# Kernel tuning notes

Hardware: AMD Instinct MI355X
Metric: run time of the kernel (lower is better)

Reference implementation:

```python
import jax, jax.numpy as jnp
import numpy as np

EMBED_DIM = 1024
NUM_HEADS = 16
HEAD_DIM = EMBED_DIM // NUM_HEADS
B, S = 2, 2048


def setup_inputs() -> dict:
    key = jax.random.key(0)
    ks = jax.random.split(key, 11)
    sc = 1.0 / np.sqrt(EMBED_DIM)
    d = {
        'query': jax.random.normal(ks[0], (B, S, EMBED_DIM), jnp.float32),
        'key': jax.random.normal(ks[1], (B, S, EMBED_DIM), jnp.float32),
        'value': jax.random.normal(ks[2], (B, S, EMBED_DIM), jnp.float32),
        'Wq': jax.random.normal(ks[3], (EMBED_DIM, EMBED_DIM), jnp.float32) * sc,
        'bq': jnp.zeros((EMBED_DIM,), jnp.float32),
        'Wk': jax.random.normal(ks[4], (EMBED_DIM, EMBED_DIM), jnp.float32) * sc,
        'bk': jnp.zeros((EMBED_DIM,), jnp.float32),
        'Wv': jax.random.normal(ks[5], (EMBED_DIM, EMBED_DIM), jnp.float32) * sc,
        'bv': jnp.zeros((EMBED_DIM,), jnp.float32),
        'Wo': jax.random.normal(ks[6], (EMBED_DIM, EMBED_DIM), jnp.float32) * sc,
        'bo': jnp.zeros((EMBED_DIM,), jnp.float32),
    }
    return d


def reference(query, key, value, Wq, bq, Wk, bk, Wv, bv, Wo, bo):
    b, s, _ = query.shape
    scale = 1.0 / np.sqrt(HEAD_DIM)
    # projections: torch Linear is x @ W.T + b
    q = (query @ Wq.T + bq).reshape(b, s, NUM_HEADS, HEAD_DIM).transpose(0, 2, 1, 3)
    k = (key @ Wk.T + bk).reshape(b, s, NUM_HEADS, HEAD_DIM).transpose(0, 2, 1, 3)
    v = (value @ Wv.T + bv).reshape(b, s, NUM_HEADS, HEAD_DIM).transpose(0, 2, 1, 3)
    scores = jnp.einsum('bhqd,bhkd->bhqk', q, k) * scale  # [B,H,S,S]
    causal = jnp.triu(jnp.ones((s, s), bool), k=1)
    scores = jnp.where(causal, -jnp.inf, scores)
    attn = jax.nn.softmax(scores, axis=-1)
    out = jnp.einsum('bhqk,bhkd->bhqd', attn, v)
    out = out.transpose(0, 2, 1, 3).reshape(b, s, EMBED_DIM)
    out = out @ Wo.T + bo
    return out, attn
```

## Files before the change

### kernel.cpp

```cpp
#include <hip/hip_runtime.h>
#include <hip/hip_bf16.h>

#define BATCH  2
#define SEQ    2048
#define EMBED  1024
#define NHEADS 16
#define HDIM   64
#define SCALE  0.125f
#define S2     0.180336880f
#define MFIX   20.0f
#define PPITCH 72

typedef __attribute__((ext_vector_type(8))) short   short8;
typedef __attribute__((ext_vector_type(4))) float   floatx4;

#if __has_builtin(__builtin_amdgcn_exp2f)
#define EXP2(x) __builtin_amdgcn_exp2f(x)
#else
#define EXP2(x) exp2f(x)
#endif

#define GLOAD_LDS(g, l) __builtin_amdgcn_global_load_lds(                      \
    (const __attribute__((address_space(1))) void*)(const void*)(g),           \
    (__attribute__((address_space(3))) void*)(void*)(l), 16, 0, 0)

__device__ __forceinline__ float bf2f(unsigned short h) {
    union { unsigned int u; float f; } v; v.u = ((unsigned int)h) << 16; return v.f;
}
__device__ __forceinline__ unsigned short f2bf(float f) {
    union { float f; unsigned int u; } v; v.f = f;
    unsigned int r = v.u + 0x7FFF + ((v.u >> 16) & 1);
    return (unsigned short)(r >> 16);
}
__device__ __forceinline__ unsigned int pack2(float lo, float hi) {
    return (unsigned int)f2bf(lo) | ((unsigned int)f2bf(hi) << 16);
}

__device__ __forceinline__ void bar_lds() {
    __builtin_amdgcn_sched_barrier(0);
    asm volatile("s_waitcnt lgkmcnt(0)" ::: "memory");
    __builtin_amdgcn_s_barrier();
    __builtin_amdgcn_sched_barrier(0);
}

__global__ __launch_bounds__(256)
void cvt_bf16(const float* __restrict__ q,  const float* __restrict__ k,
              const float* __restrict__ v,  const float* __restrict__ wq,
              const float* __restrict__ wk, const float* __restrict__ wv,
              const float* __restrict__ wo,
              unsigned short* __restrict__ dq,  unsigned short* __restrict__ dk,
              unsigned short* __restrict__ dv,  unsigned short* __restrict__ dwq,
              unsigned short* __restrict__ dwk, unsigned short* __restrict__ dwv,
              unsigned short* __restrict__ dwo)
{
    const float* s; unsigned short* d; int n;
    switch (blockIdx.y) {
        case 0: s = q;  d = dq;  n = BATCH * SEQ * EMBED; break;
        case 1: s = k;  d = dk;  n = BATCH * SEQ * EMBED; break;
        case 2: s = v;  d = dv;  n = BATCH * SEQ * EMBED; break;
        case 3: s = wq; d = dwq; n = EMBED * EMBED; break;
        case 4: s = wk; d = dwk; n = EMBED * EMBED; break;
        case 5: s = wv; d = dwv; n = EMBED * EMBED; break;
        default: s = wo; d = dwo; n = EMBED * EMBED; break;
    }
    const int i = (blockIdx.x * 256 + threadIdx.x) * 8;
    if (i >= n) return;
    float4 f0 = ((const float4*)(s + i))[0];
    float4 f1 = ((const float4*)(s + i))[1];
    uint4 u = {pack2(f0.x, f0.y), pack2(f0.z, f0.w),
               pack2(f1.x, f1.y), pack2(f1.z, f1.w)};
    *(uint4*)(d + i) = u;
}

__device__ __forceinline__ void gemm_body(
    const unsigned short* __restrict__ A,
    const unsigned short* __restrict__ W,
    const float* __restrict__ bias,
    void* __restrict__ Cout, const int f32out,
    const int bx, const int by)
{
    constexpr int N = EMBED;
    constexpr int K = EMBED;

    __shared__ unsigned short As[2][128 * 64];
    __shared__ unsigned short Bs[2][64 * 64];

    const int t    = threadIdx.x;
    const int w    = t >> 6;
    const int lane = t & 63;
    const int lr   = lane & 15;
    const int quad = lane >> 4;
    const int n0   = bx * 64;
    const int m0   = by * 128;

    size_t agoff[4];
    #pragma unroll
    for (int i = 0; i < 4; ++i) {
        const int slot = i * 256 + w * 64 + lane;
        const int row  = slot >> 3;
        const int g    = (slot & 7) ^ (row & 7);
        agoff[i] = (size_t)(m0 + row) * K + g * 8;
    }
    size_t bgoff[2];
    #pragma unroll
    for (int i = 0; i < 2; ++i) {
        const int slot = i * 256 + w * 64 + lane;
        const int row  = slot >> 3;
        const int g    = (slot & 7) ^ (row & 7);
        bgoff[i] = (size_t)(n0 + row) * K + g * 8;
    }

    int aoff[2][2], boff[4][2];
    #pragma unroll
    for (int mb = 0; mb < 2; ++mb)
        #pragma unroll
        for (int s = 0; s < 2; ++s) {
            const int row = w * 32 + mb * 16 + lr;
            aoff[mb][s] = row * 64 + (((s * 4 + quad) ^ (row & 7)) * 8);
        }
    #pragma unroll
    for (int nb = 0; nb < 4; ++nb)
        #pragma unroll
        for (int s = 0; s < 2; ++s) {
            const int row = nb * 16 + lr;
            boff[nb][s] = row * 64 + (((s * 4 + quad) ^ (row & 7)) * 8);
        }

    floatx4 acc[2][4];
    #pragma unroll
    for (int mb = 0; mb < 2; ++mb)
        #pragma unroll
        for (int nb = 0; nb < 4; ++nb) acc[mb][nb] = (floatx4){0.f, 0.f, 0.f, 0.f};

    auto stage = [&](int buf, int k0) {
        #pragma unroll
        for (int i = 0; i < 4; ++i)
            GLOAD_LDS(A + agoff[i] + k0, &As[buf][(i * 256 + w * 64) * 8]);
        #pragma unroll
        for (int i = 0; i < 2; ++i)
            GLOAD_LDS(W + bgoff[i] + k0, &Bs[buf][(i * 256 + w * 64) * 8]);
    };
    auto compute = [&](int buf) {
        const unsigned short* Ab = As[buf];
        const unsigned short* Bb = Bs[buf];
        #pragma unroll
        for (int s = 0; s < 2; ++s) {
            short8 a0 = *(const short8*)&Ab[aoff[0][s]];
            short8 a1 = *(const short8*)&Ab[aoff[1][s]];
            #pragma unroll
            for (int nb = 0; nb < 4; ++nb) {
                short8 bfr = *(const short8*)&Bb[boff[nb][s]];
                acc[0][nb] = __builtin_amdgcn_mfma_f32_16x16x32_bf16(a0, bfr, acc[0][nb], 0, 0, 0);
                acc[1][nb] = __builtin_amdgcn_mfma_f32_16x16x32_bf16(a1, bfr, acc[1][nb], 0, 0, 0);
            }
        }
    };

    stage(0, 0);
    __syncthreads();
    for (int k0 = 0; k0 < K; k0 += 128) {
        if (k0 + 64 < K) stage(1, k0 + 64);
        compute(0);
        __syncthreads();
        if (k0 + 128 < K) stage(0, k0 + 128);
        compute(1);
        __syncthreads();
    }

    #pragma unroll
    for (int mb = 0; mb < 2; ++mb)
        #pragma unroll
        for (int nb = 0; nb < 4; ++nb) {
            const int col = n0 + nb * 16 + lr;
            const float bv = bias[col];
            #pragma unroll
            for (int r = 0; r < 4; ++r) {
                const int row = m0 + w * 32 + mb * 16 + quad * 4 + r;
                const float val = acc[mb][nb][r] + bv;
                if (f32out) ((float*)Cout)[(size_t)row * N + col] = val;
                else        ((unsigned short*)Cout)[(size_t)row * N + col] = f2bf(val);
            }
        }
}

__global__ __launch_bounds__(256)
void gemm_qkv(const unsigned short* __restrict__ xq, const unsigned short* __restrict__ xk,
              const unsigned short* __restrict__ xv,
              const unsigned short* __restrict__ wq, const unsigned short* __restrict__ wk,
              const unsigned short* __restrict__ wv,
              const float* __restrict__ bq, const float* __restrict__ bk,
              const float* __restrict__ bv,
              unsigned short* __restrict__ Qb, unsigned short* __restrict__ Kb,
              unsigned short* __restrict__ Vb)
{
    const unsigned short *A, *W; const float* bias; unsigned short* C;
    switch (blockIdx.z) {
        case 0:  A = xq; W = wq; bias = bq; C = Qb; break;
        case 1:  A = xk; W = wk; bias = bk; C = Kb; break;
        default: A = xv; W = wv; bias = bv; C = Vb; break;
    }
    gemm_body(A, W, bias, C, 0, blockIdx.x, blockIdx.y);
}

__global__ __launch_bounds__(256)
void attn_pass(const unsigned short* __restrict__ Qb,
               const unsigned short* __restrict__ Kb,
               const unsigned short* __restrict__ Vb,
               unsigned short* __restrict__ Pb,
               float* __restrict__ Lbuf,
               unsigned short* __restrict__ AO)
{
    __shared__ unsigned short Ks[2][64][PPITCH];
    __shared__ unsigned short Vt[2][64][PPITCH];
    __shared__ unsigned short Ps[64][PPITCH];

    const int t    = threadIdx.x;
    const int w    = t >> 6;
    const int lane = t & 63;
    const int lr   = lane & 15;
    const int quad = lane >> 4;
    const int h    = blockIdx.y;
    const int b    = blockIdx.z;
    const int slot = (h >> 3) + 2 * b;
    const int qt   = (slot & 1) ? (SEQ / 64 - 1 - (int)blockIdx.x) : (int)blockIdx.x;
    const int q0   = qt * 64;
    const int srow = t >> 2;
    const int sseg = (t & 3) * 16;
    const int bh   = b * NHEADS + h;

    const size_t kvbase = (size_t)b * SEQ * EMBED + h * HDIM;

    const unsigned short* qrow = Qb + kvbase + (size_t)(q0 + w * 16 + lr) * EMBED + quad * 8;
    const short8 af0 = *(const short8*)(qrow);
    const short8 af1 = *(const short8*)(qrow + 32);

    const unsigned short* Krow = Kb + kvbase + (size_t)srow * EMBED + sseg;
    const unsigned short* Vrow = Vb + kvbase + (size_t)lane * EMBED;

    uint4 kA0, kA1, vA0, vA1;
    uint4 kB0, kB1, vB0, vB1;

    kA0 = ((const uint4*)Krow)[0];
    kA1 = ((const uint4*)Krow)[1];
    vA0 = *(const uint4*)(Vrow + w * 8);
    vA1 = *(const uint4*)(Vrow + (w + 4) * 8);
    *(uint4*)&Ks[0][srow][sseg]     = kA0;
    *(uint4*)&Ks[0][srow][sseg + 8] = kA1;
    {
        const unsigned short* p0 = (const unsigned short*)&vA0;
        const unsigned short* p1 = (const unsigned short*)&vA1;
        #pragma unroll
        for (int j = 0; j < 8; ++j) Vt[0][w * 8 + j][lane]       = p0[j];
        #pragma unroll
        for (int j = 0; j < 8; ++j) Vt[0][(w + 4) * 8 + j][lane] = p1[j];
    }
    if (qt > 0) {
        const unsigned short* kp = Krow + (size_t)64 * EMBED;
        kB0 = ((const uint4*)kp)[0];
        kB1 = ((const uint4*)kp)[1];
        vB0 = *(const uint4*)(Vrow + (size_t)64 * EMBED + w * 8);
        vB1 = *(const uint4*)(Vrow + (size_t)64 * EMBED + (w + 4) * 8);
    }
    bar_lds();

    float lsum[4];
    #pragma unroll
    for (int r = 0; r < 4; ++r) lsum[r] = 0.f;
    floatx4 of[4];
    #pragma unroll
    for (int i = 0; i < 4; ++i) of[i] = (floatx4){0.f, 0.f, 0.f, 0.f};

    unsigned short* pb_bh = Pb + (size_t)bh * SEQ * (SEQ * 2);
    const int rrow = lane >> 2;
    const int rseg = (lane & 3) * 16;

    for (int kt = 0; kt <= qt; ++kt) {
        const int c  = kt & 1;
        const int k0 = kt * 64;

        if (kt < qt) {
            if ((kt & 1) == 0) {
                *(uint4*)&Ks[c ^ 1][srow][sseg]     = kB0;
                *(uint4*)&Ks[c ^ 1][srow][sseg + 8] = kB1;
                const unsigned short* p0 = (const unsigned short*)&vB0;
                const unsigned short* p1 = (const unsigned short*)&vB1;
                #pragma unroll
                for (int j = 0; j < 8; ++j) Vt[c ^ 1][w * 8 + j][lane]       = p0[j];
                #pragma unroll
                for (int j = 0; j < 8; ++j) Vt[c ^ 1][(w + 4) * 8 + j][lane] = p1[j];
                if (kt + 2 <= qt) {
                    const unsigned short* kp = Krow + (size_t)(k0 + 128) * EMBED;
                    kA0 = ((const uint4*)kp)[0];
                    kA1 = ((const uint4*)kp)[1];
                    vA0 = *(const uint4*)(Vrow + (size_t)(k0 + 128) * EMBED + w * 8);
                    vA1 = *(const uint4*)(Vrow + (size_t)(k0 + 128) * EMBED + (w + 4) * 8);
                }
            } else {
                *(uint4*)&Ks[c ^ 1][srow][sseg]     = kA0;
                *(uint4*)&Ks[c ^ 1][srow][sseg + 8] = kA1;
                const unsigned short* p0 = (const unsigned short*)&vA0;
                const unsigned short* p1 = (const unsigned short*)&vA1;
                #pragma unroll
                for (int j = 0; j < 8; ++j) Vt[c ^ 1][w * 8 + j][lane]       = p0[j];
                #pragma unroll
                for (int j = 0; j < 8; ++j) Vt[c ^ 1][(w + 4) * 8 + j][lane] = p1[j];
                if (kt + 2 <= qt) {
                    const unsigned short* kp = Krow + (size_t)(k0 + 128) * EMBED;
                    kB0 = ((const uint4*)kp)[0];
                    kB1 = ((const uint4*)kp)[1];
                    vB0 = *(const uint4*)(Vrow + (size_t)(k0 + 128) * EMBED + w * 8);
                    vB1 = *(const uint4*)(Vrow + (size_t)(k0 + 128) * EMBED + (w + 4) * 8);
                }
            }
        }

        floatx4 sf[4];
        #pragma unroll
        for (int i = 0; i < 4; ++i) sf[i] = (floatx4){0.f, 0.f, 0.f, 0.f};
        #pragma unroll
        for (int nb = 0; nb < 4; ++nb) {
            short8 bf0 = *(const short8*)&Ks[c][nb * 16 + lr][quad * 8];
            sf[nb] = __builtin_amdgcn_mfma_f32_16x16x32_bf16(af0, bf0, sf[nb], 0, 0, 0);
        }
        #pragma unroll
        for (int nb = 0; nb < 4; ++nb) {
            short8 bf1 = *(const short8*)&Ks[c][nb * 16 + lr][32 + quad * 8];
            sf[nb] = __builtin_amdgcn_mfma_f32_16x16x32_bf16(af1, bf1, sf[nb], 0, 0, 0);
        }

        if (kt < qt) {
            #pragma unroll
            for (int nb = 0; nb < 4; ++nb)
                #pragma unroll
                for (int r = 0; r < 4; ++r) {
                    float p = EXP2(sf[nb][r] * S2 - MFIX);
                    lsum[r] += p;
                    Ps[w * 16 + quad * 4 + r][nb * 16 + lr] = f2bf(p);
                }
        } else {
            #pragma unroll
            for (int nb = 0; nb < 4; ++nb) {
                const int k = nb * 16 + lr;
                #pragma unroll
                for (int r = 0; r < 4; ++r) {
                    const int q = w * 16 + quad * 4 + r;
                    float p = 0.f;
                    if (k <= q) { p = EXP2(sf[nb][r] * S2 - MFIX); lsum[r] += p; }
                    Ps[w * 16 + quad * 4 + r][nb * 16 + lr] = f2bf(p);
                }
            }
        }

        {
            const unsigned short* ps = &Ps[w * 16 + rrow][rseg];
            unsigned short* op = pb_bh + (size_t)(q0 + w * 16 + rrow) * (SEQ * 2) + k0 + rseg;
            *(uint4*)op       = *(const uint4*)ps;
            *(uint4*)(op + 8) = *(const uint4*)(ps + 8);
        }

        #pragma unroll
        for (int ss = 0; ss < 2; ++ss) {
            short8 paf = *(const short8*)&Ps[w * 16 + lr][ss * 32 + quad * 8];
            #pragma unroll
            for (int nb = 0; nb < 4; ++nb) {
                short8 vf = *(const short8*)&Vt[c][nb * 16 + lr][ss * 32 + quad * 8];
                of[nb] = __builtin_amdgcn_mfma_f32_16x16x32_bf16(paf, vf, of[nb], 0, 0, 0);
            }
        }

        bar_lds();
    }

    float invl[4];
    #pragma unroll
    for (int r = 0; r < 4; ++r) {
        #pragma unroll
        for (int off = 1; off < 16; off <<= 1)
            lsum[r] += __shfl_xor(lsum[r], off, 64);
        invl[r] = 1.f / lsum[r];
    }
    if (lr == 0) {
        #pragma unroll
        for (int r = 0; r < 4; ++r)
            Lbuf[(size_t)bh * SEQ + q0 + w * 16 + quad * 4 + r] = invl[r];
    }

    #pragma unroll
    for (int nb = 0; nb < 4; ++nb)
        #pragma unroll
        for (int r = 0; r < 4; ++r)
            Ps[w * 16 + quad * 4 + r][nb * 16 + lr] = f2bf(of[nb][r] * invl[r]);
    {
        unsigned short* ao = AO + (size_t)(b * SEQ + q0 + w * 16 + rrow) * EMBED + h * HDIM + rseg;
        *(uint4*)ao       = *(const uint4*)&Ps[w * 16 + rrow][rseg];
        *(uint4*)(ao + 8) = *(const uint4*)&Ps[w * 16 + rrow][rseg + 8];
    }
}

__global__ __launch_bounds__(256)
void out_norm(const unsigned short* __restrict__ AO, const unsigned short* __restrict__ Wo16,
              const float* __restrict__ bo, float* __restrict__ out,
              float* __restrict__ attn, const float* __restrict__ Lbuf)
{
    const int id = blockIdx.x;
    if (id < 512) {
        gemm_body(AO, Wo16, bo, out, 1, id & 15, id >> 4);
        return;
    }
    const int id2   = id - 512;
    const int bh    = id2 >> 5;
    const int x     = id2 & 31;
    const int chunk = (bh & 1) ? (31 - x) : x;
    const int t     = threadIdx.x;
    const int w     = t >> 6;
    const int lane  = t & 63;

    const unsigned short* pb = (const unsigned short*)(attn + (size_t)bh * SEQ * SEQ);
    float* ab = attn + (size_t)bh * SEQ * SEQ;

    for (int i = 0; i < 16; ++i) {
        const int q  = chunk * 64 + w * 16 + i;
        const int qc = (q & ~63) + 64;
        const float il = Lbuf[(size_t)bh * SEQ + q];
        const unsigned short* src = pb + (size_t)q * (SEQ * 2);
        float* dst = ab + (size_t)q * SEQ;

        uint4 rr[4];
        #pragma unroll
        for (int s = 0; s < 4; ++s) {
            const int c = lane * 8 + s * 512;
            if (c < qc) rr[s] = *(const uint4*)(src + c);
        }
        #pragma unroll
        for (int s = 0; s < 4; ++s) {
            const int c = lane * 8 + s * 512;
            if (c < qc) {
                const unsigned short* u = (const unsigned short*)&rr[s];
                float4 f0 = {bf2f(u[0]) * il, bf2f(u[1]) * il, bf2f(u[2]) * il, bf2f(u[3]) * il};
                float4 f1 = {bf2f(u[4]) * il, bf2f(u[5]) * il, bf2f(u[6]) * il, bf2f(u[7]) * il};
                ((float4*)(dst + c))[0] = f0;
                ((float4*)(dst + c))[1] = f1;
            }
        }
        for (int c = qc + lane * 8; c < SEQ; c += 512) {
            float4 z = {0.f, 0.f, 0.f, 0.f};
            ((float4*)(dst + c))[0] = z;
            ((float4*)(dst + c))[1] = z;
        }
    }
}

extern "C" void kernel_launch(void* const* d_in, const int* in_sizes, int n_in,
                              void* d_out, int out_size, void* d_ws, size_t ws_size,
                              hipStream_t stream)
{
    const float* query = (const float*)d_in[0];
    const float* key   = (const float*)d_in[1];
    const float* value = (const float*)d_in[2];
    const float* Wq    = (const float*)d_in[3];
    const float* bq    = (const float*)d_in[4];
    const float* Wk    = (const float*)d_in[5];
    const float* bk    = (const float*)d_in[6];
    const float* Wv    = (const float*)d_in[7];
    const float* bv    = (const float*)d_in[8];
    const float* Wo    = (const float*)d_in[9];
    const float* bo    = (const float*)d_in[10];

    float* out  = (float*)d_out;
    float* attn = out + (size_t)BATCH * SEQ * EMBED;

    const size_t tsz = (size_t)BATCH * SEQ * EMBED;
    const size_t wsz = (size_t)EMBED * EMBED;
    unsigned short* p = (unsigned short*)d_ws;
    unsigned short* xq  = p;  p += tsz;
    unsigned short* xk  = p;  p += tsz;
    unsigned short* xv  = p;  p += tsz;
    unsigned short* wq16 = p; p += wsz;
    unsigned short* wk16 = p; p += wsz;
    unsigned short* wv16 = p; p += wsz;
    unsigned short* wo16 = p; p += wsz;
    unsigned short* Qb  = p;  p += tsz;
    unsigned short* Kb  = p;  p += tsz;
    unsigned short* Vb  = p;  p += tsz;
    unsigned short* AO  = p;  p += tsz;

    float* Lbuf = (float*)xq;

    const dim3 blk(256);

    cvt_bf16<<<dim3(2048, 7), blk, 0, stream>>>(query, key, value, Wq, Wk, Wv, Wo,
                                                xq, xk, xv, wq16, wk16, wv16, wo16);

    const dim3 gqkv(EMBED / 64, (BATCH * SEQ) / 128, 3);
    gemm_qkv<<<gqkv, blk, 0, stream>>>(xq, xk, xv, wq16, wk16, wv16,
                                       bq, bk, bv, Qb, Kb, Vb);

    attn_pass<<<dim3(SEQ / 64, NHEADS, BATCH), blk, 0, stream>>>(
        Qb, Kb, Vb, (unsigned short*)attn, Lbuf, AO);

    out_norm<<<dim3(512 + 1024), blk, 0, stream>>>(AO, wo16, bo, out, attn, Lbuf);
}
```

Baseline: 832.0 us.

## Enlarge GEMM tile to 128x128 with 2x2 warp layout, drop double buffering

The shared GEMM body moves from a 128x64 tile to a 128x128 tile. Each wave now computes a 64x64 sub-tile with 4x4 MFMA accumulators, which raises arithmetic intensity per LDS load and halves the number of GEMM blocks in both the QKV and output projections. In exchange it drops the double-buffered LDS pipeline in favour of a single buffer with two barriers per k-step, so global loads no longer overlap compute. It also uses more accumulator registers and launches fewer blocks, which could hurt occupancy and the grid-level balance with the attention normalisation blocks.

Measured after the change: 836.4 us. No clear change (+0.5%).

```diff
diff --git a/kernel.cpp b/kernel.cpp
--- a/kernel.cpp
+++ b/kernel.cpp
@@ -82,100 +82,85 @@
     constexpr int N = EMBED;
     constexpr int K = EMBED;
 
-    __shared__ unsigned short As[2][128 * 64];
-    __shared__ unsigned short Bs[2][64 * 64];
+    __shared__ unsigned short As[128 * 64];
+    __shared__ unsigned short Bs[128 * 64];
 
     const int t    = threadIdx.x;
     const int w    = t >> 6;
     const int lane = t & 63;
     const int lr   = lane & 15;
     const int quad = lane >> 4;
-    const int n0   = bx * 64;
+    const int wr   = w >> 1;
+    const int wc   = w & 1;
+    const int n0   = bx * 128;
     const int m0   = by * 128;
 
-    size_t agoff[4];
+    size_t agoff[4], bgoff[4];
     #pragma unroll
     for (int i = 0; i < 4; ++i) {
-        const int slot = i * 256 + w * 64 + lane;
+        const int slot = i * 256 + t;
         const int row  = slot >> 3;
         const int g    = (slot & 7) ^ (row & 7);
         agoff[i] = (size_t)(m0 + row) * K + g * 8;
-    }
-    size_t bgoff[2];
-    #pragma unroll
-    for (int i = 0; i < 2; ++i) {
-        const int slot = i * 256 + w * 64 + lane;
-        const int row  = slot >> 3;
-        const int g    = (slot & 7) ^ (row & 7);
         bgoff[i] = (size_t)(n0 + row) * K + g * 8;
     }
 
-    int aoff[2][2], boff[4][2];
-    #pragma unroll
-    for (int mb = 0; mb < 2; ++mb)
+    int aoff[4][2], boff[4][2];
+    #pragma unroll
+    for (int mb = 0; mb < 4; ++mb)
         #pragma unroll
         for (int s = 0; s < 2; ++s) {
-            const int row = w * 32 + mb * 16 + lr;
+            const int row = wr * 64 + mb * 16 + lr;
             aoff[mb][s] = row * 64 + (((s * 4 + quad) ^ (row & 7)) * 8);
         }
     #pragma unroll
     for (int nb = 0; nb < 4; ++nb)
         #pragma unroll
         for (int s = 0; s < 2; ++s) {
-            const int row = nb * 16 + lr;
+            const int row = wc * 64 + nb * 16 + lr;
             boff[nb][s] = row * 64 + (((s * 4 + quad) ^ (row & 7)) * 8);
         }
 
-    floatx4 acc[2][4];
-    #pragma unroll
-    for (int mb = 0; mb < 2; ++mb)
+    floatx4 acc[4][4];
+    #pragma unroll
+    for (int mb = 0; mb < 4; ++mb)
         #pragma unroll
         for (int nb = 0; nb < 4; ++nb) acc[mb][nb] = (floatx4){0.f, 0.f, 0.f, 0.f};
 
-    auto stage = [&](int buf, int k0) {
+    for (int k0 = 0; k0 < K; k0 += 64) {
+        __syncthreads();
         #pragma unroll
         for (int i = 0; i < 4; ++i)
-            GLOAD_LDS(A + agoff[i] + k0, &As[buf][(i * 256 + w * 64) * 8]);
-        #pragma unroll
-        for (int i = 0; i < 2; ++i)
-            GLOAD_LDS(W + bgoff[i] + k0, &Bs[buf][(i * 256 + w * 64) * 8]);
-    };
-    auto compute = [&](int buf) {
-        const unsigned short* Ab = As[buf];
-        const unsigned short* Bb = Bs[buf];
+            GLOAD_LDS(A + agoff[i] + k0, &As[(i * 256 + w * 64) * 8]);
+        #pragma unroll
+        for (int i = 0; i < 4; ++i)
+            GLOAD_LDS(W + bgoff[i] + k0, &Bs[(i * 256 + w * 64) * 8]);
+        __syncthreads();
+
         #pragma unroll
         for (int s = 0; s < 2; ++s) {
-            short8 a0 = *(const short8*)&Ab[aoff[0][s]];
-            short8 a1 = *(const short8*)&Ab[aoff[1][s]];
-            #pragma unroll
-            for (int nb = 0; nb < 4; ++nb) {
-                short8 bfr = *(const short8*)&Bb[boff[nb][s]];
-                acc[0][nb] = __builtin_amdgcn_mfma_f32_16x16x32_bf16(a0, bfr, acc[0][nb], 0, 0, 0);
-                acc[1][nb] = __builtin_amdgcn_mfma_f32_16x16x32_bf16(a1, bfr, acc[1][nb], 0, 0, 0);
-            }
-        }
-    };
-
-    stage(0, 0);
-    __syncthreads();
-    for (int k0 = 0; k0 < K; k0 += 128) {
-        if (k0 + 64 < K) stage(1, k0 + 64);
-        compute(0);
-        __syncthreads();
-        if (k0 + 128 < K) stage(0, k0 + 128);
-        compute(1);
-        __syncthreads();
-    }
-
-    #pragma unroll
-    for (int mb = 0; mb < 2; ++mb)
+            short8 av[4], bv[4];
+            #pragma unroll
+            for (int mb = 0; mb < 4; ++mb) av[mb] = *(const short8*)&As[aoff[mb][s]];
+            #pragma unroll
+            for (int nb = 0; nb < 4; ++nb) bv[nb] = *(const short8*)&Bs[boff[nb][s]];
+            #pragma unroll
+            for (int mb = 0; mb < 4; ++mb)
+                #pragma unroll
+                for (int nb = 0; nb < 4; ++nb)
+                    acc[mb][nb] = __builtin_amdgcn_mfma_f32_16x16x32_bf16(av[mb], bv[nb], acc[mb][nb], 0, 0, 0);
+        }
+    }
+
+    #pragma unroll
+    for (int mb = 0; mb < 4; ++mb)
         #pragma unroll
         for (int nb = 0; nb < 4; ++nb) {
-            const int col = n0 + nb * 16 + lr;
+            const int col = n0 + wc * 64 + nb * 16 + lr;
             const float bv = bias[col];
             #pragma unroll
             for (int r = 0; r < 4; ++r) {
-                const int row = m0 + w * 32 + mb * 16 + quad * 4 + r;
+                const int row = m0 + wr * 64 + mb * 16 + quad * 4 + r;
                 const float val = acc[mb][nb][r] + bv;
                 if (f32out) ((float*)Cout)[(size_t)row * N + col] = val;
                 else        ((unsigned short*)Cout)[(size_t)row * N + col] = f2bf(val);
@@ -403,11 +388,11 @@
               float* __restrict__ attn, const float* __restrict__ Lbuf)
 {
     const int id = blockIdx.x;
-    if (id < 512) {
-        gemm_body(AO, Wo16, bo, out, 1, id & 15, id >> 4);
+    if (id < 256) {
+        gemm_body(AO, Wo16, bo, out, 1, id & 7, id >> 3);
         return;
     }
-    const int id2   = id - 512;
+    const int id2   = id - 256;
     const int bh    = id2 >> 5;
     const int x     = id2 & 31;
     const int chunk = (bh & 1) ? (31 - x) : x;
@@ -491,12 +476,12 @@
     cvt_bf16<<<dim3(2048, 7), blk, 0, stream>>>(query, key, value, Wq, Wk, Wv, Wo,
                                                 xq, xk, xv, wq16, wk16, wv16, wo16);
 
-    const dim3 gqkv(EMBED / 64, (BATCH * SEQ) / 128, 3);
+    const dim3 gqkv(EMBED / 128, (BATCH * SEQ) / 128, 3);
     gemm_qkv<<<gqkv, blk, 0, stream>>>(xq, xk, xv, wq16, wk16, wv16,
                                        bq, bk, bv, Qb, Kb, Vb);
 
     attn_pass<<<dim3(SEQ / 64, NHEADS, BATCH), blk, 0, stream>>>(
         Qb, Kb, Vb, (unsigned short*)attn, Lbuf, AO);
 
-    out_norm<<<dim3(512 + 1024), blk, 0, stream>>>(AO, wo16, bo, out, attn, Lbuf);
-}
+    out_norm<<<dim3(256 + 1024), blk, 0, stream>>>(AO, wo16, bo, out, attn, Lbuf);
+}
```
